# Kernel optimization log

Hardware: AMD Instinct MI355X
Metric: run time of the kernel (lower is better)

Reference implementation:

```python
import jax, jax.numpy as jnp
import numpy as np
from jax import lax

R = 3                      # blob_r
S = 2 * R + 1              # 7: maxpool / neighborhood kernel size
THRESH = 0.997
PS_XY = 0.1                # vs_xy
PS_Z = 0.02                # vs_z
ZMIN = -2.0                # zrange[0]
K_PEAKS = 131072           # static upper bound replacing torch.nonzero

_offs = np.arange(S)
_gz, _gy, _gx = np.meshgrid(_offs, _offs, _offs, indexing='ij')  # patch axis order [z,y,x]
GZ = jnp.asarray(_gz.ravel(), dtype=jnp.int32)
GY = jnp.asarray(_gy.ravel(), dtype=jnp.int32)
GX = jnp.asarray(_gx.ravel(), dtype=jnp.int32)
# centroid filters: offsets -r..r along the matching patch axis (matches torch meshgrid layout)
FZ = jnp.asarray((_gz.ravel() - R).astype(np.float32))
FY = jnp.asarray((_gy.ravel() - R).astype(np.float32))
FX = jnp.asarray((_gx.ravel() - R).astype(np.float32))


def setup_inputs() -> dict:
    key = jax.random.key(0)
    pred_vol = jax.random.uniform(key, (1, 1, 128, 512, 512), dtype=jnp.float32)
    return {"pred_vol": pred_vol, "max_peaks": K_PEAKS}


def _forward(pred_vol, max_peaks):
    vol = pred_vol[0, 0]                               # [D,H,W]
    D, H, W = vol.shape
    thr = jnp.where(vol > THRESH, vol, 0.0)
    # MaxPool3d(kernel=2r+1, stride=1, padding=r) == SAME max window (pad with -inf)
    mp = lax.reduce_window(thr, -jnp.inf, lax.max, (S, S, S), (1, 1, 1), [(R, R)] * 3)
    conf = jnp.where((mp > 0.0) & (mp == thr), mp, 0.0)  # local maxima above threshold
    # fixed-size peak extraction (replaces torch.nonzero); zero-valued entries are padding
    vals, idx = lax.top_k(conf.reshape(-1), max_peaks)   # [K], [K]
    z = idx // (H * W)
    y = (idx % (H * W)) // W
    x = idx % W
    padv = jnp.pad(vol, R)                               # ConstantPad3d(r, 0)
    # gather (2r+1)^3 neighborhoods around each peak: [K, S^3]
    patches = padv[z[:, None] + GZ[None, :], y[:, None] + GY[None, :], x[:, None] + GX[None, :]]
    s0 = patches.sum(axis=1)                             # conv3d with ones filter == conf_rec sum
    xloc = jnp.einsum('kp,p->k', patches, FX) / s0
    yloc = jnp.einsum('kp,p->k', patches, FY) / s0
    zloc = jnp.einsum('kp,p->k', patches, FZ) / s0
    xf = x.astype(jnp.float32)
    yf = y.astype(jnp.float32)
    zf = z.astype(jnp.float32)
    xrec = (xf + xloc - (W - 1) / 2.0) * PS_XY
    yrec = (yf + yloc - (H - 1) / 2.0) * PS_XY
    zrec = (zf + zloc + 0.5) * PS_Z + ZMIN
    valid = vals > 0.0
    xyz = jnp.where(valid[:, None], jnp.stack((xrec, yrec, zrec), axis=1), 0.0)  # [K,3]
    out = jnp.concatenate([xyz, vals[:, None]], axis=1)  # [K,4] = (x,y,z,conf), padded rows are 0
    return out, valid


def reference(pred_vol, max_peaks):
    return _forward(pred_vol, max_peaks)
```

## Files before the change

kernel.cpp:

```cpp
#include <hip/hip_runtime.h>

#define DD 128
#define HH 512
#define WW 512
#define NVOX (DD*HH*WW)
#define THRESHV 0.997f
#define KPEAKS 131072
#define PEAK_CAP (1u<<18)
#define NBINS 65536


__global__ void k_init(unsigned* counters, unsigned* hist) {
    unsigned t = blockIdx.x * 1024u + threadIdx.x;
    if (t < 64) counters[t] = 0u;
    if (t < NBINS) hist[t] = 0u;
}

__global__ void k_find(const float4* __restrict__ vol4, const float* __restrict__ vol,
                       unsigned* counters, unsigned* hist,
                       unsigned long long* keys, float4* psums) {
    __shared__ unsigned lcnt, pcnt, lbase;
    __shared__ unsigned cidx[1024];
    __shared__ unsigned long long lbuf[512];
    __shared__ float4 sbuf[512];
    if (threadIdx.x == 0) { lcnt = 0; pcnt = 0; }
    __syncthreads();

    unsigned base4 = blockIdx.x * 8192u + threadIdx.x;
    float4 v[8];
#pragma unroll
    for (int i = 0; i < 8; i++) v[i] = vol4[base4 + i * 1024u];
    unsigned m = 0u;
#pragma unroll
    for (int i = 0; i < 8; i++) {
        m |= (v[i].x > THRESHV ? 1u : 0u) << (4 * i);
        m |= (v[i].y > THRESHV ? 1u : 0u) << (4 * i + 1);
        m |= (v[i].z > THRESHV ? 1u : 0u) << (4 * i + 2);
        m |= (v[i].w > THRESHV ? 1u : 0u) << (4 * i + 3);
    }
    while (m) {
        int b = __ffs(m) - 1;
        m &= m - 1u;
        unsigned f4 = base4 + (unsigned)(b >> 2) * 1024u;
        cidx[atomicAdd(&lcnt, 1u) & 1023u] = f4 * 4u + (unsigned)(b & 3);
    }
    __syncthreads();

    unsigned n = lcnt > 1024u ? 1024u : lcnt;
    int lane = threadIdx.x & 63;
    int wv = threadIdx.x >> 6;
    int dz = lane / 7, dy = lane - dz * 7;
    for (unsigned base = (unsigned)wv * 2u; base < n; base += 32u) {
        bool has2 = (base + 1u < n);
        unsigned idxA = cidx[base];
        unsigned idxB = has2 ? cidx[base + 1u] : idxA;
        int zA = idxA >> 18, yA = (idxA >> 9) & 511, xA = idxA & 511;
        int zB = idxB >> 18, yB = (idxB >> 9) & 511, xB = idxB & 511;
        int nzA = zA + dz - 3, nyA = yA + dy - 3;
        int nzB = zB + dz - 3, nyB = yB + dy - 3;
        bool rowokA = (lane < 49) && ((unsigned)nzA < DD) && ((unsigned)nyA < HH);
        bool rowokB = (lane < 49) && ((unsigned)nzB < DD) && ((unsigned)nyB < HH);
        size_t rbA = rowokA ? (((size_t)(unsigned)nzA << 18) | ((size_t)(unsigned)nyA << 9))
                            : (((size_t)zA << 18) | ((size_t)yA << 9));
        size_t rbB = rowokB ? (((size_t)(unsigned)nzB << 18) | ((size_t)(unsigned)nyB << 9))
                            : (((size_t)zB << 18) | ((size_t)yB << 9));
        float rvA[7], rvB[7];
        bool intAB = (xA >= 3) && (xA <= WW - 4) && (xB >= 3) && (xB <= WW - 4);
        if (intAB) {
            float4 fA0 = *(const float4*)(vol + rbA + (unsigned)(xA - 3));
            float4 fA1 = *(const float4*)(vol + rbA + (unsigned)(xA + 1));
            float4 fB0 = *(const float4*)(vol + rbB + (unsigned)(xB - 3));
            float4 fB1 = *(const float4*)(vol + rbB + (unsigned)(xB + 1));
            rvA[0] = fA0.x; rvA[1] = fA0.y; rvA[2] = fA0.z; rvA[3] = fA0.w;
            rvA[4] = fA1.x; rvA[5] = fA1.y; rvA[6] = fA1.z;
            rvB[0] = fB0.x; rvB[1] = fB0.y; rvB[2] = fB0.z; rvB[3] = fB0.w;
            rvB[4] = fB1.x; rvB[5] = fB1.y; rvB[6] = fB1.z;
        } else {
#pragma unroll
            for (int d = 0; d < 7; d++) {
                int nxA = xA + d - 3;
                bool okA = (unsigned)nxA < WW;
                float va = vol[rbA + (unsigned)(okA ? nxA : xA)];
                rvA[d] = okA ? va : 0.f;
                int nxB = xB + d - 3;
                bool okB = (unsigned)nxB < WW;
                float vb = vol[rbB + (unsigned)(okB ? nxB : xB)];
                rvB[d] = okB ? vb : 0.f;
            }
        }
        if (!rowokA) {
#pragma unroll
            for (int d = 0; d < 7; d++) rvA[d] = 0.f;
        }
        if (!rowokB) {
#pragma unroll
            for (int d = 0; d < 7; d++) rvB[d] = 0.f;
        }
        float centerA = __shfl(rvA[3], 24);
        float centerB = __shfl(rvB[3], 24);

        {
            bool kill = false;
            float s0r = 0.f, sxr = 0.f;
#pragma unroll
            for (int d = 0; d < 7; d++) {
                kill |= rvA[d] > centerA;
                s0r += rvA[d];
                sxr += rvA[d] * (float)(d - 3);
            }
            if (!__any(kill)) {
                float s0 = s0r, sx = sxr;
                float sy = s0r * (float)(dy - 3);
                float sz = s0r * (float)(dz - 3);
                for (int off = 32; off; off >>= 1) {
                    s0 += __shfl_down(s0, off);
                    sx += __shfl_down(sx, off);
                    sy += __shfl_down(sy, off);
                    sz += __shfl_down(sz, off);
                }
                if (lane == 0) {
                    unsigned bits = __float_as_uint(centerA);
                    atomicAdd(&hist[(~bits) & 0xFFFFu], 1u);
                    unsigned li = atomicAdd(&pcnt, 1u);
                    if (li < 512u) {
                        lbuf[li] = ((unsigned long long)bits << 32) | idxA;
                        sbuf[li] = make_float4(s0, sx, sy, sz);
                    }
                }
            }
        }
        if (has2) {
            bool kill = false;
            float s0r = 0.f, sxr = 0.f;
#pragma unroll
            for (int d = 0; d < 7; d++) {
                kill |= rvB[d] > centerB;
                s0r += rvB[d];
                sxr += rvB[d] * (float)(d - 3);
            }
            if (!__any(kill)) {
                float s0 = s0r, sx = sxr;
                float sy = s0r * (float)(dy - 3);
                float sz = s0r * (float)(dz - 3);
                for (int off = 32; off; off >>= 1) {
                    s0 += __shfl_down(s0, off);
                    sx += __shfl_down(sx, off);
                    sy += __shfl_down(sy, off);
                    sz += __shfl_down(sz, off);
                }
                if (lane == 0) {
                    unsigned bits = __float_as_uint(centerB);
                    atomicAdd(&hist[(~bits) & 0xFFFFu], 1u);
                    unsigned li = atomicAdd(&pcnt, 1u);
                    if (li < 512u) {
                        lbuf[li] = ((unsigned long long)bits << 32) | idxB;
                        sbuf[li] = make_float4(s0, sx, sy, sz);
                    }
                }
            }
        }
    }
    __syncthreads();
    if (threadIdx.x == 0) lbase = atomicAdd(&counters[1], pcnt);
    __syncthreads();
    unsigned np = pcnt > 512u ? 512u : pcnt;
    for (unsigned i = threadIdx.x; i < np; i += 1024u) {
        unsigned p = lbase + i;
        if (p < PEAK_CAP) { keys[p] = lbuf[i]; psums[p] = sbuf[i]; }
    }
}

__global__ void k_scan(const unsigned* __restrict__ hist, unsigned* cursor) {
    __shared__ unsigned partial[1024];
    int t = threadIdx.x;
    const uint4* h4 = (const uint4*)(hist + t * 64);
    uint4 loc[16];
#pragma unroll
    for (int i = 0; i < 16; i++) loc[i] = h4[i];
    unsigned s = 0;
#pragma unroll
    for (int i = 0; i < 16; i++) s += loc[i].x + loc[i].y + loc[i].z + loc[i].w;
    partial[t] = s;
    __syncthreads();
    for (int off = 1; off < 1024; off <<= 1) {
        unsigned v = (t >= off) ? partial[t - off] : 0u;
        __syncthreads();
        partial[t] += v;
        __syncthreads();
    }
    unsigned run = (t == 0) ? 0u : partial[t - 1];
    uint4* c4 = (uint4*)(cursor + t * 64);
#pragma unroll
    for (int i = 0; i < 16; i++) {
        uint4 h = loc[i]; uint4 o;
        o.x = run; run += h.x;
        o.y = run; run += h.y;
        o.z = run; run += h.z;
        o.w = run; run += h.w;
        c4[i] = o;
    }
}

__global__ void k_scatter(const unsigned* __restrict__ counters,
                          const unsigned long long* __restrict__ keys,
                          unsigned* cursor, unsigned long long* sorted,
                          unsigned* sslot,
                          float4* __restrict__ out, float* __restrict__ valid) {
    unsigned np = counters[1]; if (np > PEAK_CAP) np = PEAK_CAP;
    unsigned t = blockIdx.x * 1024u + threadIdx.x;
    if (t < np) {
        unsigned long long key = keys[t];
        unsigned bits = (unsigned)(key >> 32);
        unsigned pos = atomicAdd(&cursor[(~bits) & 0xFFFFu], 1u);
        if (pos < PEAK_CAP) { sorted[pos] = key; sslot[pos] = t; }
    } else if (t < KPEAKS) {
        out[t] = make_float4(0.f, 0.f, 0.f, 0.f);
        valid[t] = 0.f;
    }
}

__global__ void k_finish(const unsigned* __restrict__ counters,
                         const unsigned long long* __restrict__ sorted,
                         const unsigned* __restrict__ sslot,
                         const float4* __restrict__ psums,
                         float4* __restrict__ out, float* __restrict__ valid) {
    unsigned np = counters[1]; if (np > PEAK_CAP) np = PEAK_CAP;
    unsigned t = blockIdx.x * 1024u + threadIdx.x;
    if (t >= np) return;
    unsigned long long key = sorted[t];
    unsigned bits = (unsigned)(key >> 32);
    unsigned s = t;
    while (s > 0 && (unsigned)(sorted[s - 1] >> 32) == bits) s--;
    unsigned myidx = (unsigned)key;
    unsigned rank = 0, e = s;
    while (e < np) {
        unsigned long long k2 = sorted[e];
        if ((unsigned)(k2 >> 32) != bits) break;
        if ((unsigned)k2 < myidx) rank++;
        e++;
    }
    unsigned row = s + rank;
    if (row >= KPEAKS) return;
    unsigned idx = myidx;
    int z = idx >> 18, y = (idx >> 9) & 511, x = idx & 511;
    float4 ps = psums[sslot[t]];
    float val = __uint_as_float(bits);
    float xloc = ps.y / ps.x, yloc = ps.z / ps.x, zloc = ps.w / ps.x;
    float xr = ((float)x + xloc - (float)(WW - 1) * 0.5f) * 0.1f;
    float yr = ((float)y + yloc - (float)(HH - 1) * 0.5f) * 0.1f;
    float zr = ((float)z + zloc + 0.5f) * 0.02f - 2.0f;
    out[row] = make_float4(xr, yr, zr, val);
    valid[row] = 1.f;
}

extern "C" void kernel_launch(void* const* d_in, const int* in_sizes, int n_in,
                              void* d_out, int out_size, void* d_ws, size_t ws_size,
                              hipStream_t stream) {
    const float* vol = (const float*)d_in[0];

    char* w = (char*)d_ws;
    unsigned* counters = (unsigned*)w;
    unsigned* hist     = (unsigned*)(w + 1024);
    unsigned* cursor   = (unsigned*)(w + 1024 + NBINS * 4);
    char* w2 = w + 1024 + 2 * NBINS * 4;
    unsigned long long* keys   = (unsigned long long*)w2;
    unsigned long long* sorted = keys + PEAK_CAP;
    unsigned* sslot = (unsigned*)(sorted + PEAK_CAP);
    float4*   psums = (float4*)(sslot + PEAK_CAP);

    float* out_rows = (float*)d_out;
    float* valid = out_rows + (size_t)KPEAKS * 4;

    k_init<<<NBINS / 1024, 1024, 0, stream>>>(counters, hist);
    k_find<<<NVOX / 32768, 1024, 0, stream>>>((const float4*)vol, vol, counters, hist, keys, psums);
    k_scan<<<1, 1024, 0, stream>>>(hist, cursor);
    k_scatter<<<PEAK_CAP / 1024, 1024, 0, stream>>>(counters, keys, cursor, sorted, sslot,
                                                    (float4*)out_rows, valid);
    k_finish<<<PEAK_CAP / 1024, 1024, 0, stream>>>(counters, sorted, sslot, psums,
                                                   (float4*)out_rows, valid);
}
```

Baseline: 264.5 us.

## Stage volume tiles into LDS via global_load_lds with smaller 512-thread blocks

```diff
diff --git a/kernel.cpp b/kernel.cpp
--- a/kernel.cpp
+++ b/kernel.cpp
@@ -16,23 +16,41 @@
     if (t < NBINS) hist[t] = 0u;
 }
 
-__global__ void k_find(const float4* __restrict__ vol4, const float* __restrict__ vol,
-                       unsigned* counters, unsigned* hist,
-                       unsigned long long* keys, float4* psums) {
+__global__ __launch_bounds__(512, 8)
+void k_find(const float4* __restrict__ vol4, const float* __restrict__ vol,
+            unsigned* counters, unsigned* hist,
+            unsigned long long* keys, float4* psums) {
+    __shared__ float4 tile[2048];
     __shared__ unsigned lcnt, pcnt, lbase;
-    __shared__ unsigned cidx[1024];
-    __shared__ unsigned long long lbuf[512];
-    __shared__ float4 sbuf[512];
+    __shared__ unsigned cidx[384];
+    __shared__ unsigned long long lbuf[192];
+    __shared__ float4 sbuf[192];
     if (threadIdx.x == 0) { lcnt = 0; pcnt = 0; }
     __syncthreads();
 
-    unsigned base4 = blockIdx.x * 8192u + threadIdx.x;
-    float4 v[8];
-#pragma unroll
-    for (int i = 0; i < 8; i++) v[i] = vol4[base4 + i * 1024u];
+    unsigned t = threadIdx.x;
+    unsigned lane = t & 63u;
+    unsigned w = t >> 6;
+    unsigned blockBase4 = blockIdx.x * 2048u;
+
+#pragma unroll
+    for (unsigned i = 0; i < 4; i++) {
+        unsigned f = i * 512u + w * 64u;
+        const float4* gp = vol4 + blockBase4 + f + lane;
+        __builtin_amdgcn_global_load_lds(
+            (const __attribute__((address_space(1))) unsigned int*)gp,
+            (__attribute__((address_space(3))) unsigned int*)(tile + f),
+            16, 0, 0);
+    }
+    __builtin_amdgcn_s_waitcnt(0);
+    __syncthreads();
+
     unsigned m = 0u;
-#pragma unroll
-    for (int i = 0; i < 8; i++) {
+    float4 v[4];
+#pragma unroll
+    for (unsigned i = 0; i < 4; i++) v[i] = tile[i * 512u + t];
+#pragma unroll
+    for (unsigned i = 0; i < 4; i++) {
         m |= (v[i].x > THRESHV ? 1u : 0u) << (4 * i);
         m |= (v[i].y > THRESHV ? 1u : 0u) << (4 * i + 1);
         m |= (v[i].z > THRESHV ? 1u : 0u) << (4 * i + 2);
@@ -41,16 +59,14 @@
     while (m) {
         int b = __ffs(m) - 1;
         m &= m - 1u;
-        unsigned f4 = base4 + (unsigned)(b >> 2) * 1024u;
-        cidx[atomicAdd(&lcnt, 1u) & 1023u] = f4 * 4u + (unsigned)(b & 3);
-    }
-    __syncthreads();
-
-    unsigned n = lcnt > 1024u ? 1024u : lcnt;
-    int lane = threadIdx.x & 63;
-    int wv = threadIdx.x >> 6;
-    int dz = lane / 7, dy = lane - dz * 7;
-    for (unsigned base = (unsigned)wv * 2u; base < n; base += 32u) {
+        unsigned f4 = blockBase4 + (unsigned)(b >> 2) * 512u + t;
+        cidx[atomicAdd(&lcnt, 1u) & 383u] = f4 * 4u + (unsigned)(b & 3);
+    }
+    __syncthreads();
+
+    unsigned n = lcnt > 384u ? 384u : lcnt;
+    int dz = (int)lane / 7, dy = (int)lane - dz * 7;
+    for (unsigned base = w * 2u; base < n; base += 16u) {
         bool has2 = (base + 1u < n);
         unsigned idxA = cidx[base];
         unsigned idxB = has2 ? cidx[base + 1u] : idxA;
@@ -122,7 +138,7 @@
                     unsigned bits = __float_as_uint(centerA);
                     atomicAdd(&hist[(~bits) & 0xFFFFu], 1u);
                     unsigned li = atomicAdd(&pcnt, 1u);
-                    if (li < 512u) {
+                    if (li < 192u) {
                         lbuf[li] = ((unsigned long long)bits << 32) | idxA;
                         sbuf[li] = make_float4(s0, sx, sy, sz);
                     }
@@ -152,7 +168,7 @@
                     unsigned bits = __float_as_uint(centerB);
                     atomicAdd(&hist[(~bits) & 0xFFFFu], 1u);
                     unsigned li = atomicAdd(&pcnt, 1u);
-                    if (li < 512u) {
+                    if (li < 192u) {
                         lbuf[li] = ((unsigned long long)bits << 32) | idxB;
                         sbuf[li] = make_float4(s0, sx, sy, sz);
                     }
@@ -163,8 +179,8 @@
     __syncthreads();
     if (threadIdx.x == 0) lbase = atomicAdd(&counters[1], pcnt);
     __syncthreads();
-    unsigned np = pcnt > 512u ? 512u : pcnt;
-    for (unsigned i = threadIdx.x; i < np; i += 1024u) {
+    unsigned np = pcnt > 192u ? 192u : pcnt;
+    for (unsigned i = threadIdx.x; i < np; i += 512u) {
         unsigned p = lbase + i;
         if (p < PEAK_CAP) { keys[p] = lbuf[i]; psums[p] = sbuf[i]; }
     }
@@ -272,7 +288,7 @@
     float* valid = out_rows + (size_t)KPEAKS * 4;
 
     k_init<<<NBINS / 1024, 1024, 0, stream>>>(counters, hist);
-    k_find<<<NVOX / 32768, 1024, 0, stream>>>((const float4*)vol, vol, counters, hist, keys, psums);
+    k_find<<<NVOX / 8192, 512, 0, stream>>>((const float4*)vol, vol, counters, hist, keys, psums);
     k_scan<<<1, 1024, 0, stream>>>(hist, cursor);
     k_scatter<<<PEAK_CAP / 1024, 1024, 0, stream>>>(counters, keys, cursor, sorted, sslot,
                                                     (float4*)out_rows, valid);
```

After: 255.0 us, median of 2. -3.6%, faster.
